# Optimization experiments

Hardware: AMD Instinct MI355X
Metric: run time of the kernel (lower is better)

## Reference

```python
import jax, jax.numpy as jnp
import numpy as np

B, S, D, H = 4, 2048, 1024, 16
DH = D // H  # 64


def setup_inputs() -> dict:
    key = jax.random.key(0)
    ks = jax.random.split(key, 8)
    sc = 1.0 / np.sqrt(D)
    return {
        "hidden_states": jax.random.normal(ks[0], (B, S, D), jnp.float32),
        "attention_mask": jnp.zeros((B, 1, 1, S), jnp.float32),
        "Wq": jax.random.normal(ks[1], (D, D), jnp.float32) * sc,
        "bq": jnp.zeros((D,), jnp.float32),
        "Wk": jax.random.normal(ks[2], (D, D), jnp.float32) * sc,
        "bk": jnp.zeros((D,), jnp.float32),
        "Wv": jax.random.normal(ks[3], (D, D), jnp.float32) * sc,
        "bv": jnp.zeros((D,), jnp.float32),
    }


def _heads(x):
    # [B,S,D] -> [B,H,S,DH]
    b, s, _ = x.shape
    return x.reshape(b, s, H, DH).transpose(0, 2, 1, 3)


def reference(hidden_states, attention_mask, Wq, bq, Wk, bk, Wv, bv):
    q = _heads(hidden_states @ Wq + bq)
    k = _heads(hidden_states @ Wk + bk)
    v = _heads(hidden_states @ Wv + bv)
    scores = jnp.einsum('bhqd,bhkd->bhqk', q, k) / jnp.sqrt(jnp.float32(DH))
    scores = scores + attention_mask  # additive mask, broadcast
    probs = jax.nn.softmax(scores, axis=-1)  # dropout is identity in eval
    out = jnp.einsum('bhqk,bhkd->bhqd', probs, v)
    b, h, s, dh = out.shape
    return out.transpose(0, 2, 1, 3).reshape(b, s, h * dh)
```

## Files before the change

kernel.cpp:

```cpp
#include <hip/hip_runtime.h>
#include <hip/hip_bf16.h>
#include <cstdint>

typedef _Float16 f16;
typedef f16 f16x8 __attribute__((ext_vector_type(8)));
typedef f16 f16x4 __attribute__((ext_vector_type(4)));
typedef float f32x4 __attribute__((ext_vector_type(4)));

#define MFMA16(a, b, c) __builtin_amdgcn_mfma_f32_16x16x32_f16((a), (b), (c), 0, 0, 0)

constexpr int Bc = 4, Sc = 2048, Dc = 1024, Hc = 16, DHc = 64;

typedef __attribute__((address_space(1))) const uint32_t gbl_u32;
typedef __attribute__((address_space(3))) uint32_t lds_u32;
__device__ __forceinline__ void gld_lds16(const void* g, void* l) {
  __builtin_amdgcn_global_load_lds((gbl_u32*)g, (lds_u32*)l, 16, 0, 0);
}

__global__ __launch_bounds__(256) void cast_w_kernel(
    const float* __restrict__ Wq, const float* __restrict__ Wk,
    const float* __restrict__ Wv, f16* __restrict__ Wt) {
  __shared__ __align__(16) f16 T[64][66];
  const int z = blockIdx.z;
  const float* W = (z == 0) ? Wq : (z == 1) ? Wk : Wv;
  const int n0 = blockIdx.x * 64, k0 = blockIdx.y * 64;
  const int t = threadIdx.x;
#pragma unroll
  for (int p = 0; p < 4; p++) {
    int idx = t + p * 256;
    int r = idx >> 4, c = idx & 15;
    float4 v = *(const float4*)(W + (size_t)(k0 + r) * Dc + n0 + c * 4);
    T[r][c * 4 + 0] = (f16)v.x;
    T[r][c * 4 + 1] = (f16)v.y;
    T[r][c * 4 + 2] = (f16)v.z;
    T[r][c * 4 + 3] = (f16)v.w;
  }
  __syncthreads();
#pragma unroll
  for (int p = 0; p < 2; p++) {
    int idx = t + p * 256;
    int n = idx >> 3, c = idx & 7;
    f16x8 tmp;
#pragma unroll
    for (int j = 0; j < 8; j++) tmp[j] = T[c * 8 + j][n];
    *(f16x8*)(Wt + ((size_t)z * Dc + n0 + n) * Dc + k0 + c * 8) = tmp;
  }
}

__global__ __launch_bounds__(256) void cast_x_kernel(const float* __restrict__ X,
                                                     f16* __restrict__ X16) {
  size_t i = ((size_t)blockIdx.x * 256 + threadIdx.x) * 8;
  float4 a = *(const float4*)(X + i);
  float4 b = *(const float4*)(X + i + 4);
  f16x8 h;
  h[0] = (f16)a.x; h[1] = (f16)a.y; h[2] = (f16)a.z; h[3] = (f16)a.w;
  h[4] = (f16)b.x; h[5] = (f16)b.y; h[6] = (f16)b.z; h[7] = (f16)b.w;
  *(f16x8*)(X16 + i) = h;
}

__global__ __launch_bounds__(256) void qkv_gemm_kernel(
    const f16* __restrict__ X16, const f16* __restrict__ Wt,
    const float* __restrict__ bq, const float* __restrict__ bk,
    const float* __restrict__ bv, f16* __restrict__ Qo, f16* __restrict__ Ko,
    f16* __restrict__ Vo) {
  const int lin = blockIdx.x;
  const int xcd = lin & 7, jj = lin >> 3;
  const int bn = jj >> 3;
  const int bm = (xcd << 3) | (jj & 7);
  const int z = bn >> 3;
  const int n0 = (bn & 7) * 128;
  const int m0 = bm * 128;
  const f16* W = Wt + (size_t)bn * 128 * Dc;
  const float* bias = (z == 0) ? bq : (z == 1) ? bk : bv;

  __shared__ __align__(16) f16 Xs[128 * 32];
  __shared__ __align__(16) f16 Ws[128 * 32];

  const int t = threadIdx.x;
  const int wave = t >> 6, lane = t & 63;
  const int l16 = lane & 15, quad = lane >> 4;
  const int wm = (wave >> 1) * 64, wn = (wave & 1) * 64;

  f32x4 acc[4][4];
#pragma unroll
  for (int i = 0; i < 4; i++)
#pragma unroll
    for (int j = 0; j < 4; j++) acc[i][j] = (f32x4){0.f, 0.f, 0.f, 0.f};

  for (int k0 = 0; k0 < Dc; k0 += 32) {
#pragma unroll
    for (int p = 0; p < 2; p++) {
      int cb = p * 256 + wave * 64;
      int chunk = cb + lane;
      int row = chunk >> 2, c8 = (chunk & 3) * 8;
      gld_lds16(X16 + (size_t)(m0 + row) * Dc + k0 + c8, (f16*)Xs + (size_t)cb * 8);
      gld_lds16(W + (size_t)row * Dc + k0 + c8, (f16*)Ws + (size_t)cb * 8);
    }
    __syncthreads();

    f16x8 aF[4], bF[4];
#pragma unroll
    for (int mt = 0; mt < 4; mt++)
      aF[mt] = *(const f16x8*)(&Xs[(wm + mt * 16 + l16) * 32 + quad * 8]);
#pragma unroll
    for (int nt = 0; nt < 4; nt++)
      bF[nt] = *(const f16x8*)(&Ws[(wn + nt * 16 + l16) * 32 + quad * 8]);
#pragma unroll
    for (int mt = 0; mt < 4; mt++)
#pragma unroll
      for (int nt = 0; nt < 4; nt++)
        acc[mt][nt] = MFMA16(aF[mt], bF[nt], acc[mt][nt]);
    __syncthreads();
  }

#pragma unroll
  for (int nt = 0; nt < 4; nt++) {
    int col = n0 + wn + nt * 16 + l16;
    float bval = bias[col];
    int h = col >> 6, d = col & 63;
    if (z == 2) {
#pragma unroll
      for (int mt = 0; mt < 4; mt++) {
        int m = m0 + wm + mt * 16 + quad * 4;
        int b = m >> 11, sbase = m & 2047;
        f16x4 pk;
#pragma unroll
        for (int r = 0; r < 4; r++) pk[r] = (f16)(acc[mt][nt][r] + bval);
        *(f16x4*)(Vo + (((size_t)(b * Hc + h)) * DHc + d) * Sc + sbase) = pk;
      }
    } else {
      const float sc = (z == 0) ? 0.18033688011112042f : 1.0f;
      f16* O = (z == 0) ? Qo : Ko;
#pragma unroll
      for (int mt = 0; mt < 4; mt++) {
#pragma unroll
        for (int r = 0; r < 4; r++) {
          int m = m0 + wm + mt * 16 + quad * 4 + r;
          int b = m >> 11, s = m & 2047;
          O[(((size_t)(b * Hc + h)) * Sc + s) * DHc + d] =
              (f16)((acc[mt][nt][r] + bval) * sc);
        }
      }
    }
  }
}

__global__ __launch_bounds__(256) void flash_kernel(
    const f16* __restrict__ Q, const f16* __restrict__ K,
    const f16* __restrict__ Vt, const float* __restrict__ mask,
    float* __restrict__ out) {
  const int lin = blockIdx.x;
  const int xcd = lin & 7, jj = lin >> 3;
  const int bh = (xcd << 3) | (jj & 7);
  const int qt = jj >> 3;
  const int b = bh >> 4, h = bh & 15;
  const int t = threadIdx.x;
  const int wave = t >> 6, lane = t & 63;
  const int l16 = lane & 15, quad = lane >> 4;
  const int qbase = qt * 128 + wave * 32;

  __shared__ __align__(16) f16 Ks[2][4096];
  __shared__ __align__(16) f16 Vs[2][4096];
  __shared__ __align__(16) float Ms[2048];

  const f16* Kb = K + (size_t)bh * Sc * DHc;
  const f16* Vb = Vt + (size_t)bh * DHc * Sc;

  constexpr float L2E = 1.44269504088896340736f;

  const int qsw8 = (quad ^ ((l16 >> 1) & 3)) * 8;

  const f16* kp[2];
  const f16* vp[2];
  int ldsOff[2];
#pragma unroll
  for (int p = 0; p < 2; p++) {
    int cb = p * 256 + wave * 64;
    int i = cb + lane;
    int half = i >> 8, row = (i >> 2) & 63, q8 = i & 3;
    int q8g = q8 ^ ((row >> 1) & 3);
    int g = (row & 32) | ((row & 12) << 1) | ((row & 16) >> 2) | (row & 3);
    kp[p] = Kb + (size_t)g * DHc + half * 32 + q8g * 8;
    vp[p] = Vb + (size_t)row * Sc + half * 32 + q8g * 8;
    ldsOff[p] = cb * 8;
  }
  auto stage = [&](int buf) {
#pragma unroll
    for (int p = 0; p < 2; p++) {
      gld_lds16(kp[p], (f16*)Ks + buf * 4096 + ldsOff[p]);
      gld_lds16(vp[p], (f16*)Vs + buf * 4096 + ldsOff[p]);
      kp[p] += 64 * DHc;
      vp[p] += 64;
    }
  };

  f16x8 qa[2][2];
#pragma unroll
  for (int mt = 0; mt < 2; mt++) {
    const f16* qb = Q + ((size_t)bh * Sc + qbase + mt * 16 + l16) * DHc;
    qa[mt][0] = *(const f16x8*)(qb + quad * 8);
    qa[mt][1] = *(const f16x8*)(qb + 32 + quad * 8);
  }

  f16x8 ones;
#pragma unroll
  for (int j = 0; j < 8; j++) ones[j] = (f16)1.0f;

  stage(0);
  {
    const float* mrow = mask + (size_t)b * Sc + t * 8;
    float4 a0 = *(const float4*)(mrow);
    float4 a1 = *(const float4*)(mrow + 4);
    f32x4 m0 = (f32x4){a0.x * L2E, a0.y * L2E, a0.z * L2E, a0.w * L2E};
    f32x4 m1 = (f32x4){a1.x * L2E, a1.y * L2E, a1.z * L2E, a1.w * L2E};
    *(f32x4*)(&Ms[t * 8]) = m0;
    *(f32x4*)(&Ms[t * 8 + 4]) = m1;
  }
  __syncthreads();

  f32x4 lacc[2];
  f32x4 o[2][4];
#pragma unroll
  for (int mt = 0; mt < 2; mt++) {
    lacc[mt] = (f32x4){0.f, 0.f, 0.f, 0.f};
#pragma unroll
    for (int dt = 0; dt < 4; dt++) o[mt][dt] = (f32x4){0.f, 0.f, 0.f, 0.f};
  }

  for (int c = 0; c < 32; c++) {
    const int buf = c & 1;
    if (c < 31) stage(buf ^ 1);

    const int mb = c * 64 + quad * 8;
    f32x4 minit[4];
    minit[0] = *(const f32x4*)(&Ms[mb + 0]);
    minit[1] = *(const f32x4*)(&Ms[mb + 4]);
    minit[2] = *(const f32x4*)(&Ms[mb + 32]);
    minit[3] = *(const f32x4*)(&Ms[mb + 36]);

    f16x8 ka[4][2];
#pragma unroll
    for (int nt = 0; nt < 4; nt++) {
      int rb = (nt * 16 + l16) * 32 + qsw8;
      ka[nt][0] = *(const f16x8*)(&Ks[buf][rb]);
      ka[nt][1] = *(const f16x8*)(&Ks[buf][2048 + rb]);
    }

    f32x4 s0[4], s1[4];
#pragma unroll
    for (int nt = 0; nt < 4; nt++) {
      f32x4 a = minit[nt];
      a = MFMA16(ka[nt][0], qa[0][0], a);
      a = MFMA16(ka[nt][1], qa[0][1], a);
      s0[nt] = a;
      f32x4 a2 = minit[nt];
      a2 = MFMA16(ka[nt][0], qa[1][0], a2);
      a2 = MFMA16(ka[nt][1], qa[1][1], a2);
      s1[nt] = a2;
    }

    f16x8 pa[2][2];
#pragma unroll
    for (int blk = 0; blk < 2; blk++) {
      f16x8 p0, p1;
#pragma unroll
      for (int half = 0; half < 2; half++) {
        int nt = blk * 2 + half;
#pragma unroll
        for (int r = 0; r < 4; r++) {
          p0[half * 4 + r] = (f16)__builtin_amdgcn_exp2f(s0[nt][r]);
          p1[half * 4 + r] = (f16)__builtin_amdgcn_exp2f(s1[nt][r]);
        }
      }
      pa[0][blk] = p0;
      pa[1][blk] = p1;
    }

    lacc[0] = MFMA16(pa[0][0], ones, lacc[0]);
    lacc[0] = MFMA16(pa[0][1], ones, lacc[0]);
    lacc[1] = MFMA16(pa[1][0], ones, lacc[1]);
    lacc[1] = MFMA16(pa[1][1], ones, lacc[1]);

#pragma unroll
    for (int dt = 0; dt < 4; dt++) {
      int rb = (dt * 16 + l16) * 32 + qsw8;
      f16x8 v0 = *(const f16x8*)(&Vs[buf][rb]);
      f16x8 v1 = *(const f16x8*)(&Vs[buf][2048 + rb]);
      o[0][dt] = MFMA16(pa[0][0], v0, o[0][dt]);
      o[0][dt] = MFMA16(pa[0][1], v1, o[0][dt]);
      o[1][dt] = MFMA16(pa[1][0], v0, o[1][dt]);
      o[1][dt] = MFMA16(pa[1][1], v1, o[1][dt]);
    }

    __syncthreads();
  }

#pragma unroll
  for (int mt = 0; mt < 2; mt++) {
    float inv[4];
#pragma unroll
    for (int r = 0; r < 4; r++) inv[r] = 1.0f / lacc[mt][r];
#pragma unroll
    for (int dt = 0; dt < 4; dt++) {
      int col = h * 64 + dt * 16 + l16;
#pragma unroll
      for (int r = 0; r < 4; r++) {
        int row = qbase + mt * 16 + quad * 4 + r;
        out[((size_t)b * Sc + row) * Dc + col] = o[mt][dt][r] * inv[r];
      }
    }
  }
}

extern "C" void kernel_launch(void* const* d_in, const int* in_sizes, int n_in,
                              void* d_out, int out_size, void* d_ws,
                              size_t ws_size, hipStream_t stream) {
  (void)in_sizes; (void)n_in; (void)out_size; (void)ws_size;
  const float* hidden = (const float*)d_in[0];
  const float* mask   = (const float*)d_in[1];
  const float* Wq     = (const float*)d_in[2];
  const float* bq     = (const float*)d_in[3];
  const float* Wk     = (const float*)d_in[4];
  const float* bk     = (const float*)d_in[5];
  const float* Wv     = (const float*)d_in[6];
  const float* bv     = (const float*)d_in[7];
  float* out = (float*)d_out;

  uint8_t* w = (uint8_t*)d_ws;
  f16* Wt   = (f16*)(w);
  f16* X16  = (f16*)(w + (size_t)6 * 1024 * 1024);
  f16* Q16  = (f16*)(w + (size_t)22 * 1024 * 1024);
  f16* K16  = (f16*)(w + (size_t)38 * 1024 * 1024);
  f16* Vt16 = (f16*)(w + (size_t)54 * 1024 * 1024);

  cast_w_kernel<<<dim3(16, 16, 3), 256, 0, stream>>>(Wq, Wk, Wv, Wt);
  cast_x_kernel<<<4096, 256, 0, stream>>>(hidden, X16);
  qkv_gemm_kernel<<<dim3(1536), 256, 0, stream>>>(X16, Wt, bq, bk, bv,
                                                  Q16, K16, Vt16);
  flash_kernel<<<dim3(1024), 256, 0, stream>>>(Q16, K16, Vt16, mask, out);
}
```

Measured before the change: 257.3 us.

## Deepen GEMM K-tile with swizzled LDS, vectorize Q/K stores, double flash query tile

```diff
diff --git a/kernel.cpp b/kernel.cpp
--- a/kernel.cpp
+++ b/kernel.cpp
@@ -72,9 +72,10 @@
   const int m0 = bm * 128;
   const f16* W = Wt + (size_t)bn * 128 * Dc;
   const float* bias = (z == 0) ? bq : (z == 1) ? bk : bv;
-
-  __shared__ __align__(16) f16 Xs[128 * 32];
-  __shared__ __align__(16) f16 Ws[128 * 32];
+  const bool zqk = (z != 2);
+
+  __shared__ __align__(16) f16 Xs[128 * 64];
+  __shared__ __align__(16) f16 Ws[128 * 64];
 
   const int t = threadIdx.x;
   const int wave = t >> 6, lane = t & 63;
@@ -87,38 +88,74 @@
 #pragma unroll
     for (int j = 0; j < 4; j++) acc[i][j] = (f32x4){0.f, 0.f, 0.f, 0.f};
 
-  for (int k0 = 0; k0 < Dc; k0 += 32) {
-#pragma unroll
-    for (int p = 0; p < 2; p++) {
-      int cb = p * 256 + wave * 64;
-      int chunk = cb + lane;
-      int row = chunk >> 2, c8 = (chunk & 3) * 8;
-      gld_lds16(X16 + (size_t)(m0 + row) * Dc + k0 + c8, (f16*)Xs + (size_t)cb * 8);
-      gld_lds16(W + (size_t)row * Dc + k0 + c8, (f16*)Ws + (size_t)cb * 8);
+  for (int k0 = 0; k0 < Dc; k0 += 64) {
+#pragma unroll
+    for (int p = 0; p < 4; p++) {
+      int i = p * 256 + wave * 64 + lane;
+      int row = i >> 3, oct = i & 7;
+      int so = (oct ^ (row & 7)) * 8;
+      gld_lds16(X16 + (size_t)(m0 + row) * Dc + k0 + so, (f16*)Xs + (size_t)i * 8);
+      gld_lds16(W + (size_t)row * Dc + k0 + so, (f16*)Ws + (size_t)i * 8);
     }
     __syncthreads();
 
-    f16x8 aF[4], bF[4];
-#pragma unroll
-    for (int mt = 0; mt < 4; mt++)
-      aF[mt] = *(const f16x8*)(&Xs[(wm + mt * 16 + l16) * 32 + quad * 8]);
-#pragma unroll
-    for (int nt = 0; nt < 4; nt++)
-      bF[nt] = *(const f16x8*)(&Ws[(wn + nt * 16 + l16) * 32 + quad * 8]);
-#pragma unroll
-    for (int mt = 0; mt < 4; mt++)
-#pragma unroll
-      for (int nt = 0; nt < 4; nt++)
-        acc[mt][nt] = MFMA16(aF[mt], bF[nt], acc[mt][nt]);
+#pragma unroll
+    for (int kk = 0; kk < 2; kk++) {
+      f16x8 aF[4], bF[4];
+#pragma unroll
+      for (int mt = 0; mt < 4; mt++) {
+        int r = wm + mt * 16 + l16;
+        aF[mt] = *(const f16x8*)(&Xs[r * 64 + (((kk * 4 + quad) ^ (r & 7)) * 8)]);
+      }
+#pragma unroll
+      for (int nt = 0; nt < 4; nt++) {
+        int r = wn + nt * 16 + l16;
+        bF[nt] = *(const f16x8*)(&Ws[r * 64 + (((kk * 4 + quad) ^ (r & 7)) * 8)]);
+      }
+      if (zqk) {
+#pragma unroll
+        for (int nt = 0; nt < 4; nt++)
+#pragma unroll
+          for (int mt = 0; mt < 4; mt++)
+            acc[nt][mt] = MFMA16(bF[nt], aF[mt], acc[nt][mt]);
+      } else {
+#pragma unroll
+        for (int mt = 0; mt < 4; mt++)
+#pragma unroll
+          for (int nt = 0; nt < 4; nt++)
+            acc[mt][nt] = MFMA16(aF[mt], bF[nt], acc[mt][nt]);
+      }
+    }
     __syncthreads();
   }
 
-#pragma unroll
-  for (int nt = 0; nt < 4; nt++) {
-    int col = n0 + wn + nt * 16 + l16;
-    float bval = bias[col];
-    int h = col >> 6, d = col & 63;
-    if (z == 2) {
+  if (zqk) {
+    f16* O = (z == 0) ? Qo : Ko;
+    const float sc = (z == 0) ? 0.18033688011112042f : 1.0f;
+    const int h = (n0 + wn) >> 6;
+#pragma unroll
+    for (int nt = 0; nt < 4; nt++) {
+      int cb = n0 + wn + nt * 16 + quad * 4;
+      float4 bv4 = *(const float4*)(bias + cb);
+      int d0 = nt * 16 + quad * 4;
+#pragma unroll
+      for (int mt = 0; mt < 4; mt++) {
+        int m = m0 + wm + mt * 16 + l16;
+        int b = m >> 11, s = m & 2047;
+        f16x4 pk;
+        pk[0] = (f16)((acc[nt][mt][0] + bv4.x) * sc);
+        pk[1] = (f16)((acc[nt][mt][1] + bv4.y) * sc);
+        pk[2] = (f16)((acc[nt][mt][2] + bv4.z) * sc);
+        pk[3] = (f16)((acc[nt][mt][3] + bv4.w) * sc);
+        *(f16x4*)(O + (((size_t)(b * Hc + h)) * Sc + s) * DHc + d0) = pk;
+      }
+    }
+  } else {
+#pragma unroll
+    for (int nt = 0; nt < 4; nt++) {
+      int col = n0 + wn + nt * 16 + l16;
+      float bval = bias[col];
+      int h = col >> 6, d = col & 63;
 #pragma unroll
       for (int mt = 0; mt < 4; mt++) {
         int m = m0 + wm + mt * 16 + quad * 4;
@@ -127,19 +164,6 @@
 #pragma unroll
         for (int r = 0; r < 4; r++) pk[r] = (f16)(acc[mt][nt][r] + bval);
         *(f16x4*)(Vo + (((size_t)(b * Hc + h)) * DHc + d) * Sc + sbase) = pk;
-      }
-    } else {
-      const float sc = (z == 0) ? 0.18033688011112042f : 1.0f;
-      f16* O = (z == 0) ? Qo : Ko;
-#pragma unroll
-      for (int mt = 0; mt < 4; mt++) {
-#pragma unroll
-        for (int r = 0; r < 4; r++) {
-          int m = m0 + wm + mt * 16 + quad * 4 + r;
-          int b = m >> 11, s = m & 2047;
-          O[(((size_t)(b * Hc + h)) * Sc + s) * DHc + d] =
-              (f16)((acc[mt][nt][r] + bval) * sc);
-        }
       }
     }
   }
@@ -157,7 +181,7 @@
   const int t = threadIdx.x;
   const int wave = t >> 6, lane = t & 63;
   const int l16 = lane & 15, quad = lane >> 4;
-  const int qbase = qt * 128 + wave * 32;
+  const int qbase = qt * 256 + wave * 64;
 
   __shared__ __align__(16) f16 Ks[2][4096];
   __shared__ __align__(16) f16 Vs[2][4096];
@@ -194,9 +218,9 @@
     }
   };
 
-  f16x8 qa[2][2];
-#pragma unroll
-  for (int mt = 0; mt < 2; mt++) {
+  f16x8 qa[4][2];
+#pragma unroll
+  for (int mt = 0; mt < 4; mt++) {
     const f16* qb = Q + ((size_t)bh * Sc + qbase + mt * 16 + l16) * DHc;
     qa[mt][0] = *(const f16x8*)(qb + quad * 8);
     qa[mt][1] = *(const f16x8*)(qb + 32 + quad * 8);
@@ -211,17 +235,15 @@
     const float* mrow = mask + (size_t)b * Sc + t * 8;
     float4 a0 = *(const float4*)(mrow);
     float4 a1 = *(const float4*)(mrow + 4);
-    f32x4 m0 = (f32x4){a0.x * L2E, a0.y * L2E, a0.z * L2E, a0.w * L2E};
-    f32x4 m1 = (f32x4){a1.x * L2E, a1.y * L2E, a1.z * L2E, a1.w * L2E};
-    *(f32x4*)(&Ms[t * 8]) = m0;
-    *(f32x4*)(&Ms[t * 8 + 4]) = m1;
+    *(f32x4*)(&Ms[t * 8]) = (f32x4){a0.x * L2E, a0.y * L2E, a0.z * L2E, a0.w * L2E};
+    *(f32x4*)(&Ms[t * 8 + 4]) = (f32x4){a1.x * L2E, a1.y * L2E, a1.z * L2E, a1.w * L2E};
   }
   __syncthreads();
 
-  f32x4 lacc[2];
-  f32x4 o[2][4];
-#pragma unroll
-  for (int mt = 0; mt < 2; mt++) {
+  f32x4 lacc[4];
+  f32x4 o[4][4];
+#pragma unroll
+  for (int mt = 0; mt < 4; mt++) {
     lacc[mt] = (f32x4){0.f, 0.f, 0.f, 0.f};
 #pragma unroll
     for (int dt = 0; dt < 4; dt++) o[mt][dt] = (f32x4){0.f, 0.f, 0.f, 0.f};
@@ -230,73 +252,58 @@
   for (int c = 0; c < 32; c++) {
     const int buf = c & 1;
     if (c < 31) stage(buf ^ 1);
-
     const int mb = c * 64 + quad * 8;
-    f32x4 minit[4];
-    minit[0] = *(const f32x4*)(&Ms[mb + 0]);
-    minit[1] = *(const f32x4*)(&Ms[mb + 4]);
-    minit[2] = *(const f32x4*)(&Ms[mb + 32]);
-    minit[3] = *(const f32x4*)(&Ms[mb + 36]);
-
-    f16x8 ka[4][2];
-#pragma unroll
-    for (int nt = 0; nt < 4; nt++) {
-      int rb = (nt * 16 + l16) * 32 + qsw8;
-      ka[nt][0] = *(const f16x8*)(&Ks[buf][rb]);
-      ka[nt][1] = *(const f16x8*)(&Ks[buf][2048 + rb]);
-    }
-
-    f32x4 s0[4], s1[4];
-#pragma unroll
-    for (int nt = 0; nt < 4; nt++) {
-      f32x4 a = minit[nt];
-      a = MFMA16(ka[nt][0], qa[0][0], a);
-      a = MFMA16(ka[nt][1], qa[0][1], a);
-      s0[nt] = a;
-      f32x4 a2 = minit[nt];
-      a2 = MFMA16(ka[nt][0], qa[1][0], a2);
-      a2 = MFMA16(ka[nt][1], qa[1][1], a2);
-      s1[nt] = a2;
-    }
-
-    f16x8 pa[2][2];
-#pragma unroll
-    for (int blk = 0; blk < 2; blk++) {
-      f16x8 p0, p1;
-#pragma unroll
-      for (int half = 0; half < 2; half++) {
-        int nt = blk * 2 + half;
-#pragma unroll
-        for (int r = 0; r < 4; r++) {
-          p0[half * 4 + r] = (f16)__builtin_amdgcn_exp2f(s0[nt][r]);
-          p1[half * 4 + r] = (f16)__builtin_amdgcn_exp2f(s1[nt][r]);
-        }
-      }
-      pa[0][blk] = p0;
-      pa[1][blk] = p1;
-    }
-
-    lacc[0] = MFMA16(pa[0][0], ones, lacc[0]);
-    lacc[0] = MFMA16(pa[0][1], ones, lacc[0]);
-    lacc[1] = MFMA16(pa[1][0], ones, lacc[1]);
-    lacc[1] = MFMA16(pa[1][1], ones, lacc[1]);
-
-#pragma unroll
-    for (int dt = 0; dt < 4; dt++) {
-      int rb = (dt * 16 + l16) * 32 + qsw8;
-      f16x8 v0 = *(const f16x8*)(&Vs[buf][rb]);
-      f16x8 v1 = *(const f16x8*)(&Vs[buf][2048 + rb]);
-      o[0][dt] = MFMA16(pa[0][0], v0, o[0][dt]);
-      o[0][dt] = MFMA16(pa[0][1], v1, o[0][dt]);
-      o[1][dt] = MFMA16(pa[1][0], v0, o[1][dt]);
-      o[1][dt] = MFMA16(pa[1][1], v1, o[1][dt]);
+
+#pragma unroll
+    for (int kb = 0; kb < 2; kb++) {
+      f32x4 mi0 = *(const f32x4*)(&Ms[mb + kb * 32]);
+      f32x4 mi1 = *(const f32x4*)(&Ms[mb + kb * 32 + 4]);
+      int rb0 = ((2 * kb) * 16 + l16) * 32 + qsw8;
+      int rb1 = ((2 * kb + 1) * 16 + l16) * 32 + qsw8;
+      f16x8 ka00 = *(const f16x8*)(&Ks[buf][rb0]);
+      f16x8 ka01 = *(const f16x8*)(&Ks[buf][2048 + rb0]);
+      f16x8 ka10 = *(const f16x8*)(&Ks[buf][rb1]);
+      f16x8 ka11 = *(const f16x8*)(&Ks[buf][2048 + rb1]);
+
+      f16x8 pa[4];
+#pragma unroll
+      for (int mt = 0; mt < 4; mt++) {
+        f32x4 s0 = mi0, s1 = mi1;
+        s0 = MFMA16(ka00, qa[mt][0], s0);
+        s0 = MFMA16(ka01, qa[mt][1], s0);
+        s1 = MFMA16(ka10, qa[mt][0], s1);
+        s1 = MFMA16(ka11, qa[mt][1], s1);
+        auto e0 = __builtin_amdgcn_cvt_pkrtz(__builtin_amdgcn_exp2f(s0[0]),
+                                             __builtin_amdgcn_exp2f(s0[1]));
+        auto e1 = __builtin_amdgcn_cvt_pkrtz(__builtin_amdgcn_exp2f(s0[2]),
+                                             __builtin_amdgcn_exp2f(s0[3]));
+        auto e2 = __builtin_amdgcn_cvt_pkrtz(__builtin_amdgcn_exp2f(s1[0]),
+                                             __builtin_amdgcn_exp2f(s1[1]));
+        auto e3 = __builtin_amdgcn_cvt_pkrtz(__builtin_amdgcn_exp2f(s1[2]),
+                                             __builtin_amdgcn_exp2f(s1[3]));
+        f16x8 p;
+        p[0] = (f16)e0[0]; p[1] = (f16)e0[1]; p[2] = (f16)e1[0]; p[3] = (f16)e1[1];
+        p[4] = (f16)e2[0]; p[5] = (f16)e2[1]; p[6] = (f16)e3[0]; p[7] = (f16)e3[1];
+        pa[mt] = p;
+        lacc[mt] = MFMA16(p, ones, lacc[mt]);
+      }
+
+#pragma unroll
+      for (int dt = 0; dt < 4; dt++) {
+        int rb = (dt * 16 + l16) * 32 + qsw8;
+        f16x8 v = *(const f16x8*)(&Vs[buf][kb * 2048 + rb]);
+        o[0][dt] = MFMA16(pa[0], v, o[0][dt]);
+        o[1][dt] = MFMA16(pa[1], v, o[1][dt]);
+        o[2][dt] = MFMA16(pa[2], v, o[2][dt]);
+        o[3][dt] = MFMA16(pa[3], v, o[3][dt]);
+      }
     }
 
     __syncthreads();
   }
 
 #pragma unroll
-  for (int mt = 0; mt < 2; mt++) {
+  for (int mt = 0; mt < 4; mt++) {
     float inv[4];
 #pragma unroll
     for (int r = 0; r < 4; r++) inv[r] = 1.0f / lacc[mt][r];
@@ -337,5 +344,5 @@
   cast_x_kernel<<<4096, 256, 0, stream>>>(hidden, X16);
   qkv_gemm_kernel<<<dim3(1536), 256, 0, stream>>>(X16, Wt, bq, bk, bv,
                                                   Q16, K16, Vt16);
-  flash_kernel<<<dim3(1024), 256, 0, stream>>>(Q16, K16, Vt16, mask, out);
-}
+  flash_kernel<<<dim3(512), 256, 0, stream>>>(Q16, K16, Vt16, mask, out);
+}
```

Result: slower. 274.0 us (+6.5%).
